# Kernel optimization log

Measured on AMD Instinct MI355X. Metric: run time of the kernel, lower is better.

## Reference

```python
import jax, jax.numpy as jnp
import numpy as np

NUM_HEADS = 12
HEAD_DIM = 64
MASKED_BIAS = -10000.0


def setup_inputs() -> dict:
    key = jax.random.key(0)
    k1, k2, k3 = jax.random.split(key, 3)
    B, S, D = 2, 2048, 768
    return {
        "hidden_states": jax.random.normal(k1, (B, S, D), dtype=jnp.float32),
        "c_attn_w": jax.random.normal(k2, (D, 3 * D), dtype=jnp.float32) * 0.02,
        "c_attn_b": jnp.zeros((3 * D,), dtype=jnp.float32),
        "c_proj_w": jax.random.normal(k3, (D, D), dtype=jnp.float32) * 0.02,
        "c_proj_b": jnp.zeros((D,), dtype=jnp.float32),
    }


def _split_heads(x, B, S):
    # [B,S,D] -> [B,H,S,hd]
    return x.reshape(B, S, NUM_HEADS, HEAD_DIM).transpose(0, 2, 1, 3)


def reference(hidden_states, c_attn_w, c_attn_b, c_proj_w, c_proj_b):
    B, S, D = hidden_states.shape
    qkv = hidden_states @ c_attn_w + c_attn_b  # [B,S,3D]
    q, k, v = jnp.split(qkv, 3, axis=-1)
    q = _split_heads(q, B, S)
    k = _split_heads(k, B, S)
    v = _split_heads(v, B, S)

    # Unfused attention: full [B,H,S,S] scores, where-based causal mask
    attn_weights = jnp.einsum("bhqd,bhkd->bhqk", q, k)
    attn_weights = attn_weights / jnp.float32(HEAD_DIM) ** 0.5
    causal_mask = jnp.tril(jnp.ones((S, S), dtype=bool))[None, None]
    attn_weights = jnp.where(causal_mask, attn_weights,
                             jnp.asarray(MASKED_BIAS, attn_weights.dtype))
    attn_weights = jax.nn.softmax(attn_weights, axis=-1)
    attn_output = jnp.einsum("bhqk,bhkd->bhqd", attn_weights, v)

    # merge heads [B,H,S,hd] -> [B,S,D]
    attn_output = attn_output.transpose(0, 2, 1, 3).reshape(B, S, D)
    attn_output = attn_output @ c_proj_w + c_proj_b
    return attn_output
```

## Files before the change

### kernel.cpp

```cpp
#include <hip/hip_runtime.h>
#include <stdint.h>


constexpr int B_  = 2;
constexpr int S_  = 2048;
constexpr int D_  = 768;
constexpr int N3D = 3 * D_;
constexpr int M_  = B_ * S_;
constexpr int NTILE = 32 * 24;
#define QSCALE 0.1803368801111f
#define FIXED_M 8.0f

typedef __bf16 bv8 __attribute__((ext_vector_type(8)));
typedef float  fv4 __attribute__((ext_vector_type(4)));
typedef unsigned short uv4 __attribute__((ext_vector_type(4)));
typedef unsigned short uv8 __attribute__((ext_vector_type(8)));

__device__ inline unsigned short f2bf(float x) {
    __bf16 b = (__bf16)x;
    return __builtin_bit_cast(unsigned short, b);
}

__device__ inline fv4 mfma16(bv8 a, bv8 b, fv4 c) {
    return __builtin_amdgcn_mfma_f32_16x16x32_bf16(a, b, c, 0, 0, 0);
}

#define GLOAD_LDS16(g, l)                                                        \
    __builtin_amdgcn_global_load_lds(                                            \
        (__attribute__((address_space(1))) void*)(g),                            \
        (__attribute__((address_space(3))) void*)(l), 16, 0, 0)

#define VMCNT4() asm volatile("s_waitcnt vmcnt(4)" ::: "memory")
#define VMCNT0() asm volatile("s_waitcnt vmcnt(0)" ::: "memory")
#define BAR()                                                                    \
    do { asm volatile("" ::: "memory"); __builtin_amdgcn_s_barrier();            \
         asm volatile("" ::: "memory"); } while (0)

__global__ __launch_bounds__(256)
void prep(const float* __restrict__ hs, const float* __restrict__ wqkv,
          const float* __restrict__ wproj, unsigned short* __restrict__ hsb,
          unsigned short* __restrict__ wqkvT, unsigned short* __restrict__ wprojT,
          int* __restrict__ cnt)
{
    __shared__ float tl[32][33];
    const int bid = blockIdx.x, t = threadIdx.x;
    if (bid == 0 && t == 0) *cnt = 0;

    if (bid < 1536) {
        const size_t i = ((size_t)bid * 256 + t) * 8;
        const float4 a = *(const float4*)&hs[i];
        const float4 b = *(const float4*)&hs[i + 4];
        uv8 o;
        o[0] = f2bf(a.x); o[1] = f2bf(a.y); o[2] = f2bf(a.z); o[3] = f2bf(a.w);
        o[4] = f2bf(b.x); o[5] = f2bf(b.y); o[6] = f2bf(b.z); o[7] = f2bf(b.w);
        *(uv8*)&hsb[i] = o;
        return;
    }

    const float* W;
    unsigned short* WT;
    int K, N, bx, by;
    if (bid < 3264) {
        W = wqkv; WT = wqkvT; K = 768; N = 2304;
        const int b2 = bid - 1536; bx = b2 % 72; by = b2 / 72;
    } else {
        W = wproj; WT = wprojT; K = 768; N = 768;
        const int b2 = bid - 3264; bx = b2 % 24; by = b2 / 24;
    }
    const int n0 = bx * 32, k0 = by * 32;
    {
        const int r = t >> 3, c = (t & 7) * 4;
        const float4 v = *(const float4*)&W[(size_t)(k0 + r) * N + n0 + c];
        tl[r][c + 0] = v.x; tl[r][c + 1] = v.y; tl[r][c + 2] = v.z; tl[r][c + 3] = v.w;
    }
    __syncthreads();
    {
        const int rn = t >> 3, ck = (t & 7) * 4;
        uv4 o;
        o[0] = f2bf(tl[ck + 0][rn]); o[1] = f2bf(tl[ck + 1][rn]);
        o[2] = f2bf(tl[ck + 2][rn]); o[3] = f2bf(tl[ck + 3][rn]);
        *(uv4*)&WT[(size_t)(n0 + rn) * K + k0 + ck] = o;
    }
}

template<bool QKV>
__global__ __launch_bounds__(256)
void gemm_bf16(const unsigned short* __restrict__ A, const unsigned short* __restrict__ BT,
               const float* __restrict__ bias, float* __restrict__ Cf,
               unsigned short* __restrict__ Qb, unsigned short* __restrict__ Kb,
               unsigned short* __restrict__ VTb, int M, int N, int K)
{
    __shared__ unsigned short smem[16384];
    unsigned short* const sA0 = smem;
    unsigned short* const sB0 = smem + 8192;

    const int t = threadIdx.x, w = t >> 6, lane = t & 63;
    const int l15 = lane & 15, l4 = lane >> 4;
    const int m0 = blockIdx.y * 128, n0 = blockIdx.x * 128;
    const int wr = w >> 1, wc = w & 1;

    fv4 acc[4][4];
#pragma unroll
    for (int i = 0; i < 4; ++i)
#pragma unroll
        for (int j = 0; j < 4; ++j) acc[i][j] = fv4{0.f, 0.f, 0.f, 0.f};

    const int r0 = w * 16 + (lane >> 2);
    const int c0 = (lane & 3) ^ ((r0 >> 1) & 3);
    const int r1 = (w + 4) * 16 + (lane >> 2);
    const int c1 = (lane & 3) ^ ((r1 >> 1) & 3);

    auto stage = [&](int buf, int k0) {
        GLOAD_LDS16(A  + (size_t)(m0 + r0) * K + k0 + c0 * 8, sA0 + buf * 4096 + w * 512);
        GLOAD_LDS16(A  + (size_t)(m0 + r1) * K + k0 + c1 * 8, sA0 + buf * 4096 + (w + 4) * 512);
        GLOAD_LDS16(BT + (size_t)(n0 + r0) * K + k0 + c0 * 8, sB0 + buf * 4096 + w * 512);
        GLOAD_LDS16(BT + (size_t)(n0 + r1) * K + k0 + c1 * 8, sB0 + buf * 4096 + (w + 4) * 512);
    };

    stage(0, 0);
    const int nt = K >> 5;
    for (int tt = 0; tt < nt; ++tt) {
        const int cur = tt & 1;
        if (tt + 1 < nt) { stage(cur ^ 1, (tt + 1) * 32); VMCNT4(); }
        else             { VMCNT0(); }
        BAR();

        bv8 af[4], bf[4];
#pragma unroll
        for (int i = 0; i < 4; ++i) {
            const int r = wr * 64 + i * 16 + l15;
            const int c = l4 ^ ((r >> 1) & 3);
            af[i] = *(const bv8*)&sA0[cur * 4096 + r * 32 + c * 8];
        }
#pragma unroll
        for (int j = 0; j < 4; ++j) {
            const int r = wc * 64 + j * 16 + l15;
            const int c = l4 ^ ((r >> 1) & 3);
            bf[j] = *(const bv8*)&sB0[cur * 4096 + r * 32 + c * 8];
        }
        __builtin_amdgcn_s_setprio(1);
#pragma unroll
        for (int i = 0; i < 4; ++i)
#pragma unroll
            for (int j = 0; j < 4; ++j)
                acc[i][j] = mfma16(af[i], bf[j], acc[i][j]);
        __builtin_amdgcn_s_setprio(0);
        BAR();
    }

    if (QKV) {
        const int sect = n0 / 768;
        const int rem0 = n0 - sect * 768;
        if (sect < 2) {
            const float qs = (sect == 0) ? QSCALE : 1.0f;
#pragma unroll
            for (int jf = 0; jf < 4; ++jf) {
                const int c = wc * 64 + jf * 16 + l15;
                const float bb = bias[n0 + c];
                const int ch = c >> 3, off = c & 7;
#pragma unroll
                for (int i = 0; i < 4; ++i) {
                    const int rb = wr * 64 + i * 16 + l4 * 4;
#pragma unroll
                    for (int reg = 0; reg < 4; ++reg) {
                        const int r = rb + reg;
                        smem[r * 128 + ((ch ^ (r & 15)) << 3) + off] =
                            f2bf((acc[i][jf][reg] + bb) * qs);
                    }
                }
            }
            __syncthreads();
            unsigned short* const dstQK = (sect == 0) ? Qb : Kb;
            const int brow = m0 >> 11, sbase = m0 & 2047, hb = rem0 >> 6;
#pragma unroll
            for (int u = 0; u < 8; ++u) {
                const int ID = t + 256 * u;
                const int s = ID >> 4, ch = ID & 15;
                const int hh = ch >> 3, dc = ch & 7;
                const uv8 v = *(const uv8*)&smem[s * 128 + ((ch ^ (s & 15)) << 3)];
                const size_t bh = (size_t)brow * 12 + hb + hh;
                *(uv8*)&dstQK[(bh * 2048 + sbase + s) * 64 + dc * 8] = v;
            }
        } else {
#pragma unroll
            for (int jf = 0; jf < 4; ++jf) {
                const int col = n0 + wc * 64 + jf * 16 + l15;
                const float bb = bias[col];
                const int rem = col - 2 * 768;
                const int hh_ = rem >> 6, d = rem & 63;
#pragma unroll
                for (int i = 0; i < 4; ++i) {
                    const int rowb = m0 + wr * 64 + i * 16 + l4 * 4;
                    const size_t bh = (size_t)(rowb >> 11) * 12 + hh_;
                    const int s0 = rowb & 2047;
                    uv4 pk;
#pragma unroll
                    for (int reg = 0; reg < 4; ++reg) pk[reg] = f2bf(acc[i][jf][reg] + bb);
                    *(uv4*)&VTb[(bh * 64 + d) * 2048 + s0] = pk;
                }
            }
        }
    } else {
#pragma unroll
        for (int jf = 0; jf < 4; ++jf) {
            const int col = n0 + wc * 64 + jf * 16 + l15;
            const float bb = bias[col];
#pragma unroll
            for (int i = 0; i < 4; ++i) {
                const int rowb = m0 + wr * 64 + i * 16 + l4 * 4;
#pragma unroll
                for (int reg = 0; reg < 4; ++reg)
                    Cf[(size_t)(rowb + reg) * N + col] = acc[i][jf][reg] + bb;
            }
        }
    }
}

__global__ __launch_bounds__(256)
void flash_mfma(const unsigned short* __restrict__ Qb, const unsigned short* __restrict__ Kb,
                const unsigned short* __restrict__ VTb, unsigned short* __restrict__ outb,
                int* __restrict__ cnt)
{
    __shared__ unsigned short sK [2][64 * 64];
    __shared__ unsigned short sVT[2][64 * 64];
    __shared__ unsigned short sP [4][16 * 64];
    __shared__ int sj;

    const int t = threadIdx.x, w = t >> 6, lane = t & 63;
    const int l15 = lane & 15, l4 = lane >> 4;

    const int sr0 = w * 8 + (lane >> 3), sc0 = (lane & 7) ^ (sr0 & 7);
    const int sr1 = (w + 4) * 8 + (lane >> 3), sc1 = (lane & 7) ^ (sr1 & 7);

    for (;;) {
        if (t == 0) sj = atomicAdd(cnt, 1);
        __syncthreads();
        const int j = sj;
        if (j >= NTILE) return;
        const int qt = 31 - j / 24;
        const int bh = j - (j / 24) * 24;
        const int b = bh / 12, h = bh - b * 12;
        const int qrow = qt * 64 + w * 16;

        const unsigned short* Kbase = Kb  + (size_t)bh * 2048 * 64;
        const unsigned short* Vbase = VTb + (size_t)bh * 64 * 2048;

        bv8 qf[2];
        {
            const unsigned short* qp = Qb + ((size_t)bh * 2048 + qrow + l15) * 64 + l4 * 8;
            qf[0] = *(const bv8*)qp;
            qf[1] = *(const bv8*)(qp + 32);
        }

        fv4 o[4];
#pragma unroll
        for (int jf = 0; jf < 4; ++jf) o[jf] = fv4{0.f, 0.f, 0.f, 0.f};
        float l_ = 0.f;

        GLOAD_LDS16(Kbase + (size_t)sr0 * 64 + sc0 * 8, &sK[0][w * 512]);
        GLOAD_LDS16(Kbase + (size_t)sr1 * 64 + sc1 * 8, &sK[0][(w + 4) * 512]);
        GLOAD_LDS16(Vbase + (size_t)sr0 * 2048 + sc0 * 8, &sVT[0][w * 512]);
        GLOAD_LDS16(Vbase + (size_t)sr1 * 2048 + sc1 * 8, &sVT[0][(w + 4) * 512]);

        for (int kt = 0; kt <= qt; ++kt) {
            const int cur = kt & 1;
            if (kt < qt) {
                const int nk = kt + 1;
                GLOAD_LDS16(Kbase + (size_t)(nk * 64 + sr0) * 64 + sc0 * 8, &sK[cur ^ 1][w * 512]);
                GLOAD_LDS16(Kbase + (size_t)(nk * 64 + sr1) * 64 + sc1 * 8, &sK[cur ^ 1][(w + 4) * 512]);
                GLOAD_LDS16(Vbase + (size_t)sr0 * 2048 + nk * 64 + sc0 * 8, &sVT[cur ^ 1][w * 512]);
                GLOAD_LDS16(Vbase + (size_t)sr1 * 2048 + nk * 64 + sc1 * 8, &sVT[cur ^ 1][(w + 4) * 512]);
                VMCNT4();
            } else VMCNT0();
            BAR();

            fv4 st[4];
            __builtin_amdgcn_s_setprio(1);
#pragma unroll
            for (int jf = 0; jf < 4; ++jf) {
                st[jf] = fv4{-FIXED_M, -FIXED_M, -FIXED_M, -FIXED_M};
                const int kr = jf * 16 + l15;
#pragma unroll
                for (int hh = 0; hh < 2; ++hh) {
                    const bv8 ka = *(const bv8*)&sK[cur][kr * 64 + (((hh * 4 + l4) ^ (kr & 7)) * 8)];
                    st[jf] = mfma16(ka, qf[hh], st[jf]);
                }
            }
            __builtin_amdgcn_s_setprio(0);

            float ps[16];
            const int qg = qrow + l15;
            if (kt == qt) {
#pragma unroll
                for (int jf = 0; jf < 4; ++jf)
#pragma unroll
                    for (int reg = 0; reg < 4; ++reg) {
                        const int kvg = kt * 64 + jf * 16 + l4 * 4 + reg;
                        ps[jf * 4 + reg] = (kvg > qg) ? -30000.f : st[jf][reg];
                    }
            } else {
#pragma unroll
                for (int jf = 0; jf < 4; ++jf)
#pragma unroll
                    for (int reg = 0; reg < 4; ++reg) ps[jf * 4 + reg] = st[jf][reg];
            }
#pragma unroll
            for (int u = 0; u < 16; ++u) {
                const float p = exp2f(ps[u]);
                ps[u] = p;
                l_ += p;
            }

#pragma unroll
            for (int jf = 0; jf < 4; ++jf) {
                uv4 pk;
#pragma unroll
                for (int reg = 0; reg < 4; ++reg) pk[reg] = f2bf(ps[jf * 4 + reg]);
                const int chunk = jf * 2 + (l4 >> 1);
                *(uv4*)&sP[w][l15 * 64 + ((chunk ^ (l15 & 7)) * 8) + (l4 & 1) * 4] = pk;
            }

            bv8 pa[2];
#pragma unroll
            for (int hh = 0; hh < 2; ++hh)
                pa[hh] = *(const bv8*)&sP[w][l15 * 64 + (((hh * 4 + l4) ^ (l15 & 7)) * 8)];
            __builtin_amdgcn_s_setprio(1);
#pragma unroll
            for (int jf = 0; jf < 4; ++jf) {
                const int dr = jf * 16 + l15;
#pragma unroll
                for (int hh = 0; hh < 2; ++hh) {
                    const bv8 vb = *(const bv8*)&sVT[cur][dr * 64 + (((hh * 4 + l4) ^ (dr & 7)) * 8)];
                    o[jf] = mfma16(pa[hh], vb, o[jf]);
                }
            }
            __builtin_amdgcn_s_setprio(0);
            BAR();
        }

        l_ += __shfl_xor(l_, 16);
        l_ += __shfl_xor(l_, 32);
        const float inv = 1.0f / l_;
        float invq[4];
#pragma unroll
        for (int reg = 0; reg < 4; ++reg) invq[reg] = __shfl(inv, l4 * 4 + reg);
#pragma unroll
        for (int jf = 0; jf < 4; ++jf)
#pragma unroll
            for (int reg = 0; reg < 4; ++reg)
                outb[(size_t)(b * S_ + qrow + l4 * 4 + reg) * D_ + h * 64 + jf * 16 + l15] =
                    f2bf(o[jf][reg] * invq[reg]);
    }
}

extern "C" void kernel_launch(void* const* d_in, const int* in_sizes, int n_in,
                              void* d_out, int out_size, void* d_ws, size_t ws_size,
                              hipStream_t stream)
{
    const float* hs    = (const float*)d_in[0];
    const float* wqkv  = (const float*)d_in[1];
    const float* bqkv  = (const float*)d_in[2];
    const float* wproj = (const float*)d_in[3];
    const float* bproj = (const float*)d_in[4];
    float* out = (float*)d_out;

    unsigned short* hsb    = (unsigned short*)d_ws;
    unsigned short* wqkvT  = hsb    + (size_t)M_ * D_;
    unsigned short* wprojT = wqkvT  + (size_t)N3D * D_;
    unsigned short* Qb     = wprojT + (size_t)D_ * D_;
    unsigned short* Kb     = Qb     + (size_t)24 * 2048 * 64;
    unsigned short* VTb    = Kb     + (size_t)24 * 2048 * 64;
    unsigned short* attnb  = VTb    + (size_t)24 * 2048 * 64;
    int* cnt = (int*)(attnb + (size_t)M_ * D_);

    prep<<<3840, 256, 0, stream>>>(hs, wqkv, wproj, hsb, wqkvT, wprojT, cnt);
    gemm_bf16<true><<<dim3(N3D / 128, M_ / 128), 256, 0, stream>>>(
        hsb, wqkvT, bqkv, nullptr, Qb, Kb, VTb, M_, N3D, D_);
    flash_mfma<<<512, 256, 0, stream>>>(Qb, Kb, VTb, attnb, cnt);
    gemm_bf16<false><<<dim3(D_ / 128, M_ / 128), 256, 0, stream>>>(
        attnb, wprojT, bproj, out, nullptr, nullptr, nullptr, M_, D_, D_);
}
```

Baseline: 170.9 us.

## Triple-buffer GEMM and attention LDS pipelines, drop trailing barrier, add XCD swizzle

Both the GEMM and flash-attention kernels move from double to triple-buffered LDS staging. Loads are issued two tiles ahead, right after the single per-iteration barrier, which lets the trailing barrier be removed. The GEMM grid becomes 1D with an XCD-aware block swizzle meant to improve L2 locality across chiplets, and the exp/sum loop in attention uses four partial accumulators. LDS use per block grows, which may cut occupancy, and dropping a barrier depends on the three-buffer distance being enough to avoid overwriting data still being read.

```diff
diff --git a/kernel.cpp b/kernel.cpp
--- a/kernel.cpp
+++ b/kernel.cpp
@@ -44,7 +44,7 @@
 {
     __shared__ float tl[32][33];
     const int bid = blockIdx.x, t = threadIdx.x;
-    if (bid == 0 && t == 0) *cnt = 0;
+    if (bid == 0 && t < 4) cnt[t] = 0;
 
     if (bid < 1536) {
         const size_t i = ((size_t)bid * 256 + t) * 8;
@@ -88,15 +88,18 @@
 void gemm_bf16(const unsigned short* __restrict__ A, const unsigned short* __restrict__ BT,
                const float* __restrict__ bias, float* __restrict__ Cf,
                unsigned short* __restrict__ Qb, unsigned short* __restrict__ Kb,
-               unsigned short* __restrict__ VTb, int M, int N, int K)
+               unsigned short* __restrict__ VTb, int M, int N, int K, int gx)
 {
-    __shared__ unsigned short smem[16384];
+    __shared__ unsigned short smem[24576];
     unsigned short* const sA0 = smem;
-    unsigned short* const sB0 = smem + 8192;
+    unsigned short* const sB0 = smem + 12288;
 
     const int t = threadIdx.x, w = t >> 6, lane = t & 63;
     const int l15 = lane & 15, l4 = lane >> 4;
-    const int m0 = blockIdx.y * 128, n0 = blockIdx.x * 128;
+    const int nwg = gridDim.x, cpx = nwg >> 3;
+    const int orig = blockIdx.x;
+    const int swz = (orig & 7) * cpx + (orig >> 3);
+    const int m0 = (swz / gx) * 128, n0 = (swz % gx) * 128;
     const int wr = w >> 1, wc = w & 1;
 
     fv4 acc[4][4];
@@ -118,12 +121,13 @@
     };
 
     stage(0, 0);
+    stage(1, 32);
     const int nt = K >> 5;
     for (int tt = 0; tt < nt; ++tt) {
-        const int cur = tt & 1;
-        if (tt + 1 < nt) { stage(cur ^ 1, (tt + 1) * 32); VMCNT4(); }
-        else             { VMCNT0(); }
+        if (tt + 1 < nt) VMCNT4(); else VMCNT0();
         BAR();
+        if (tt + 2 < nt) stage((tt + 2) % 3, (tt + 2) * 32);
+        const int cur = tt % 3;
 
         bv8 af[4], bf[4];
 #pragma unroll
@@ -145,13 +149,13 @@
             for (int j = 0; j < 4; ++j)
                 acc[i][j] = mfma16(af[i], bf[j], acc[i][j]);
         __builtin_amdgcn_s_setprio(0);
-        BAR();
     }
 
     if (QKV) {
         const int sect = n0 / 768;
         const int rem0 = n0 - sect * 768;
         if (sect < 2) {
+            __syncthreads();
             const float qs = (sect == 0) ? QSCALE : 1.0f;
 #pragma unroll
             for (int jf = 0; jf < 4; ++jf) {
@@ -221,8 +225,8 @@
                 const unsigned short* __restrict__ VTb, unsigned short* __restrict__ outb,
                 int* __restrict__ cnt)
 {
-    __shared__ unsigned short sK [2][64 * 64];
-    __shared__ unsigned short sVT[2][64 * 64];
+    __shared__ unsigned short sK [3][64 * 64];
+    __shared__ unsigned short sVT[3][64 * 64];
     __shared__ unsigned short sP [4][16 * 64];
     __shared__ int sj;
 
@@ -245,6 +249,13 @@
         const unsigned short* Kbase = Kb  + (size_t)bh * 2048 * 64;
         const unsigned short* Vbase = VTb + (size_t)bh * 64 * 2048;
 
+        auto stage = [&](int buf, int kt) {
+            GLOAD_LDS16(Kbase + (size_t)(kt * 64 + sr0) * 64 + sc0 * 8, &sK[buf][w * 512]);
+            GLOAD_LDS16(Kbase + (size_t)(kt * 64 + sr1) * 64 + sc1 * 8, &sK[buf][(w + 4) * 512]);
+            GLOAD_LDS16(Vbase + (size_t)sr0 * 2048 + kt * 64 + sc0 * 8, &sVT[buf][w * 512]);
+            GLOAD_LDS16(Vbase + (size_t)sr1 * 2048 + kt * 64 + sc1 * 8, &sVT[buf][(w + 4) * 512]);
+        };
+
         bv8 qf[2];
         {
             const unsigned short* qp = Qb + ((size_t)bh * 2048 + qrow + l15) * 64 + l4 * 8;
@@ -257,22 +268,14 @@
         for (int jf = 0; jf < 4; ++jf) o[jf] = fv4{0.f, 0.f, 0.f, 0.f};
         float l_ = 0.f;
 
-        GLOAD_LDS16(Kbase + (size_t)sr0 * 64 + sc0 * 8, &sK[0][w * 512]);
-        GLOAD_LDS16(Kbase + (size_t)sr1 * 64 + sc1 * 8, &sK[0][(w + 4) * 512]);
-        GLOAD_LDS16(Vbase + (size_t)sr0 * 2048 + sc0 * 8, &sVT[0][w * 512]);
-        GLOAD_LDS16(Vbase + (size_t)sr1 * 2048 + sc1 * 8, &sVT[0][(w + 4) * 512]);
+        stage(0, 0);
+        if (qt >= 1) stage(1, 1);
 
         for (int kt = 0; kt <= qt; ++kt) {
-            const int cur = kt & 1;
-            if (kt < qt) {
-                const int nk = kt + 1;
-                GLOAD_LDS16(Kbase + (size_t)(nk * 64 + sr0) * 64 + sc0 * 8, &sK[cur ^ 1][w * 512]);
-                GLOAD_LDS16(Kbase + (size_t)(nk * 64 + sr1) * 64 + sc1 * 8, &sK[cur ^ 1][(w + 4) * 512]);
-                GLOAD_LDS16(Vbase + (size_t)sr0 * 2048 + nk * 64 + sc0 * 8, &sVT[cur ^ 1][w * 512]);
-                GLOAD_LDS16(Vbase + (size_t)sr1 * 2048 + nk * 64 + sc1 * 8, &sVT[cur ^ 1][(w + 4) * 512]);
-                VMCNT4();
-            } else VMCNT0();
+            if (kt < qt) VMCNT4(); else VMCNT0();
             BAR();
+            if (kt + 2 <= qt) stage((kt + 2) % 3, kt + 2);
+            const int cur = kt % 3;
 
             fv4 st[4];
             __builtin_amdgcn_s_setprio(1);
@@ -304,12 +307,15 @@
 #pragma unroll
                     for (int reg = 0; reg < 4; ++reg) ps[jf * 4 + reg] = st[jf][reg];
             }
-#pragma unroll
-            for (int u = 0; u < 16; ++u) {
-                const float p = exp2f(ps[u]);
-                ps[u] = p;
-                l_ += p;
-            }
+            float la0 = 0.f, la1 = 0.f, la2 = 0.f, la3 = 0.f;
+#pragma unroll
+            for (int u = 0; u < 16; u += 4) {
+                const float p0 = exp2f(ps[u + 0]); ps[u + 0] = p0; la0 += p0;
+                const float p1 = exp2f(ps[u + 1]); ps[u + 1] = p1; la1 += p1;
+                const float p2 = exp2f(ps[u + 2]); ps[u + 2] = p2; la2 += p2;
+                const float p3 = exp2f(ps[u + 3]); ps[u + 3] = p3; la3 += p3;
+            }
+            l_ += (la0 + la1) + (la2 + la3);
 
 #pragma unroll
             for (int jf = 0; jf < 4; ++jf) {
@@ -335,7 +341,6 @@
                 }
             }
             __builtin_amdgcn_s_setprio(0);
-            BAR();
         }
 
         l_ += __shfl_xor(l_, 16);
@@ -374,9 +379,9 @@
     int* cnt = (int*)(attnb + (size_t)M_ * D_);
 
     prep<<<3840, 256, 0, stream>>>(hs, wqkv, wproj, hsb, wqkvT, wprojT, cnt);
-    gemm_bf16<true><<<dim3(N3D / 128, M_ / 128), 256, 0, stream>>>(
-        hsb, wqkvT, bqkv, nullptr, Qb, Kb, VTb, M_, N3D, D_);
+    gemm_bf16<true><<<(N3D / 128) * (M_ / 128), 256, 0, stream>>>(
+        hsb, wqkvT, bqkv, nullptr, Qb, Kb, VTb, M_, N3D, D_, N3D / 128);
     flash_mfma<<<512, 256, 0, stream>>>(Qb, Kb, VTb, attnb, cnt);
-    gemm_bf16<false><<<dim3(D_ / 128, M_ / 128), 256, 0, stream>>>(
-        attnb, wprojT, bproj, out, nullptr, nullptr, nullptr, M_, D_, D_);
-}
+    gemm_bf16<false><<<(D_ / 128) * (M_ / 128), 256, 0, stream>>>(
+        attnb, wprojT, bproj, out, nullptr, nullptr, nullptr, M_, D_, D_, D_ / 128);
+}
```

After: 163.8 us. 1.04x faster.
